# Kernel optimization log

Measured on AMD Instinct MI355X. Metric: run time of the kernel, lower is better.

Reference implementation:

```python
import jax, jax.numpy as jnp
import numpy as np

B, Q, DIM, HEADS, HEAD_DIM, KV = 32, 4, 2048, 16, 128, 8192


def setup_inputs() -> dict:
    key = jax.random.key(0)
    ks = jax.random.split(key, 9)
    s = 0.02
    return {
        'x': jax.random.normal(ks[0], (B, Q, DIM), jnp.float32),
        'attn_bias': jax.random.normal(ks[1], (B, HEADS, Q, KV), jnp.float32),
        'cache_k': jax.random.normal(ks[2], (B, KV, HEAD_DIM), jnp.float32),
        'cache_v': jax.random.normal(ks[3], (B, KV, HEAD_DIM), jnp.float32),
        'wq': jax.random.normal(ks[4], (DIM, HEADS, HEAD_DIM), jnp.float32) * s,
        'bq': jnp.zeros((HEADS, HEAD_DIM), jnp.float32),
        'wk': jax.random.normal(ks[5], (DIM, HEAD_DIM), jnp.float32) * s,
        'bk': jnp.zeros((HEAD_DIM,), jnp.float32),
        'wv': jax.random.normal(ks[6], (DIM, HEAD_DIM), jnp.float32) * s,
        'bv': jnp.zeros((HEAD_DIM,), jnp.float32),
        'wo': jax.random.normal(ks[7], (HEADS, HEAD_DIM, DIM), jnp.float32) * s,
        'bo': jnp.zeros((DIM,), jnp.float32),
    }


def reference(x, attn_bias, cache_k, cache_v, wq, bq, wk, bk, wv, bv, wo, bo):
    q_len = x.shape[1]
    # projections (MQA: shared single-head K/V)
    q = jnp.einsum('bqd,dhe->bqhe', x, wq) + bq          # [B,Q,H,hd]
    k_new = x @ wk + bk                                   # [B,Q,hd]
    v_new = x @ wv + bv
    # rolling KV cache update: shift left by q_len, write new tokens at end
    k = jnp.roll(cache_k, -q_len, axis=1).at[:, -q_len:].set(k_new)  # [B,KV,hd]
    v = jnp.roll(cache_v, -q_len, axis=1).at[:, -q_len:].set(v_new)
    scale = 1.0 / (k.shape[-1] ** 0.5)
    p = jnp.einsum('bqhe,bke->bhqk', q, k) * scale        # [B,H,Q,KV]
    a = jax.nn.softmax(p + attn_bias, axis=-1)
    o = jnp.einsum('bhqk,bke->bqhe', a, v)                # [B,Q,H,hd]
    return jnp.einsum('bqhe,hed->bqd', o, wo) + bo        # [B,Q,DIM]
```

## Files before the change

kernel.cpp:

```cpp
#include <hip/hip_runtime.h>
#include <cstddef>
#include <cstdint>

#define BATCH 32
#define QL 4
#define DIM 2048
#define NH 16
#define HD 128
#define KVLEN 8192
#define HQ 64
#define CHUNK 512
#define NCK 16
#define KT 64
#define NT 8

typedef __attribute__((ext_vector_type(8))) short bf16x8;
typedef __attribute__((ext_vector_type(4))) float f32x4;

__device__ __forceinline__ unsigned short cvt_bf16(float f) {
    unsigned int u = __builtin_bit_cast(unsigned int, f);
    u += 0x7fffu + ((u >> 16) & 1u);
    return (unsigned short)(u >> 16);
}
__device__ __forceinline__ unsigned int pack2(float a, float b) {
    return (unsigned int)cvt_bf16(a) | ((unsigned int)cvt_bf16(b) << 16);
}
__device__ __forceinline__ float bf16_to_f32(unsigned short s) {
    unsigned int u = ((unsigned int)s) << 16;
    return __builtin_bit_cast(float, u);
}
__device__ __forceinline__ bf16x8 mk_frag(unsigned int a, unsigned int b,
                                          unsigned int c, unsigned int d) {
    unsigned int t[4] = {a, b, c, d};
    return *(const bf16x8*)t;
}

template<int VARIANT>
__global__ __launch_bounds__(256) void gemm_kernel(
    const float* __restrict__ A,
    const float* __restrict__ w0p, const float* __restrict__ w1p,
    const float* __restrict__ w2p,
    const float* __restrict__ b0p, const float* __restrict__ b1p,
    const float* __restrict__ b2p,
    float* __restrict__ o0, float* __restrict__ o1, float* __restrict__ o2)
{
    const int n0 = blockIdx.x * 64;
    const int m0 = blockIdx.y * 64;
    const int tid = threadIdx.x;
    const int wave = tid >> 6, lane = tid & 63;
    const int l15 = lane & 15, quad = lane >> 4;

    const float* W; const float* Bv; int ldw, nc;
    if (VARIANT == 0) {
        if (n0 >= 2176)      { W = w2p; Bv = b2p; ldw = 128;  nc = n0 - 2176; }
        else if (n0 >= 2048) { W = w1p; Bv = b1p; ldw = 128;  nc = n0 - 2048; }
        else                 { W = w0p; Bv = b0p; ldw = 2048; nc = n0; }
    } else { W = w0p; Bv = b0p; ldw = 2048; nc = n0; }

    __shared__ alignas(16) unsigned short a_s[64][72];
    __shared__ alignas(16) unsigned short w_s[64][68];

    const int wn = tid & 63;
    const int wk0 = (tid >> 6) * 4;

    f32x4 acc[4];
    #pragma unroll
    for (int nt = 0; nt < 4; ++nt) acc[nt] = (f32x4){0.f, 0.f, 0.f, 0.f};

    float4 apre[4];
    float wpre[4][4];

    #pragma unroll
    for (int ii = 0; ii < 4; ++ii) {
        int f = tid + 256 * ii, r = f >> 4, c4 = (f & 15) << 2;
        apre[ii] = *(const float4*)&A[(size_t)(m0 + r) * DIM + c4];
    }
    #pragma unroll
    for (int sub = 0; sub < 4; ++sub) {
        int k0 = wk0 + 16 * sub;
        const float* wp = W + (size_t)k0 * ldw + nc + wn;
        #pragma unroll
        for (int j = 0; j < 4; ++j) wpre[sub][j] = wp[(size_t)j * ldw];
    }

    for (int it = 0; it < 32; ++it) {
        __syncthreads();
        #pragma unroll
        for (int ii = 0; ii < 4; ++ii) {
            int f = tid + 256 * ii, r = f >> 4, c4 = (f & 15) << 2;
            *(uint2*)&a_s[r][c4] =
                make_uint2(pack2(apre[ii].x, apre[ii].y), pack2(apre[ii].z, apre[ii].w));
        }
        #pragma unroll
        for (int sub = 0; sub < 4; ++sub) {
            int k0 = wk0 + 16 * sub;
            *(uint2*)&w_s[wn][k0] =
                make_uint2(pack2(wpre[sub][0], wpre[sub][1]),
                           pack2(wpre[sub][2], wpre[sub][3]));
        }
        __syncthreads();
        if (it + 1 < 32) {
            const int kb = (it + 1) * 64;
            #pragma unroll
            for (int ii = 0; ii < 4; ++ii) {
                int f = tid + 256 * ii, r = f >> 4, c4 = (f & 15) << 2;
                apre[ii] = *(const float4*)&A[(size_t)(m0 + r) * DIM + kb + c4];
            }
            #pragma unroll
            for (int sub = 0; sub < 4; ++sub) {
                int k0 = kb + wk0 + 16 * sub;
                const float* wp = W + (size_t)k0 * ldw + nc + wn;
                #pragma unroll
                for (int j = 0; j < 4; ++j) wpre[sub][j] = wp[(size_t)j * ldw];
            }
        }
        #pragma unroll
        for (int kf = 0; kf < 2; ++kf) {
            bf16x8 af = *(const bf16x8*)&a_s[16 * wave + l15][kf * 32 + quad * 8];
            #pragma unroll
            for (int nt = 0; nt < 4; ++nt) {
                uint2 lo = *(const uint2*)&w_s[nt * 16 + l15][kf * 32 + quad * 8];
                uint2 hi = *(const uint2*)&w_s[nt * 16 + l15][kf * 32 + quad * 8 + 4];
                bf16x8 wf = mk_frag(lo.x, lo.y, hi.x, hi.y);
                acc[nt] = __builtin_amdgcn_mfma_f32_16x16x32_bf16(af, wf, acc[nt], 0, 0, 0);
            }
        }
    }
    #pragma unroll
    for (int nt = 0; nt < 4; ++nt)
        #pragma unroll
        for (int reg = 0; reg < 4; ++reg) {
            int row = m0 + 16 * wave + quad * 4 + reg;
            int col = n0 + nt * 16 + l15;
            float s = acc[nt][reg];
            if (VARIANT == 1) {
                o0[(size_t)row * DIM + col] = s + Bv[col];
            } else {
                int b = row >> 2, q = row & 3;
                if (col < 2048) {
                    int h = col >> 7, e = col & 127;
                    o0[((size_t)(b * 64 + h * 4 + q)) * 128 + e] = s + b0p[col];
                } else if (col < 2176) {
                    int e = col - 2048;
                    o1[(size_t)row * 128 + e] = s + b1p[e];
                } else {
                    int e = col - 2176;
                    o2[(size_t)row * 128 + e] = s + b2p[e];
                }
            }
        }
}

__global__ __launch_bounds__(256, 2) void attn_kernel(
    const float* __restrict__ qws, const float* __restrict__ kws,
    const float* __restrict__ vws,
    const float* __restrict__ cachek, const float* __restrict__ cachev,
    const float* __restrict__ abias,
    float* __restrict__ opart, float* __restrict__ lpart)
{
    const int ck = blockIdx.x;
    const int b  = blockIdx.y;
    const int tid = threadIdx.x;
    const int wave = tid >> 6, lane = tid & 63;
    const int l15 = lane & 15, quad = lane >> 4;
    const float scale = 0.08838834764831845f;

    __shared__ alignas(16) unsigned short k_s[KT][136];
    __shared__ alignas(16) unsigned short v_sT[HD][68];
    __shared__ alignas(16) unsigned short p_s[4][16][72];

    bf16x8 qf[4];
    {
        const float* qrow = qws + ((size_t)b * HQ + 16 * wave + l15) * HD;
        #pragma unroll
        for (int kf = 0; kf < 4; ++kf) {
            float4 f0 = *(const float4*)&qrow[kf * 32 + quad * 8];
            float4 f1 = *(const float4*)&qrow[kf * 32 + quad * 8 + 4];
            qf[kf] = mk_frag(pack2(f0.x, f0.y), pack2(f0.z, f0.w),
                             pack2(f1.x, f1.y), pack2(f1.z, f1.w));
        }
    }

    const int kbase0 = ck * CHUNK;
    const int ve = tid & 127;
    const int vkq = (tid >> 7);

    const float* bptr[4];
    #pragma unroll
    for (int reg = 0; reg < 4; ++reg) {
        int hq = 16 * wave + quad * 4 + reg;
        int h = hq >> 2, q = hq & 3;
        bptr[reg] = abias + (((size_t)(b * NH + h)) * QL + q) * KVLEN + kbase0 + l15;
    }

    float4 kpre[8];
    float vpre[8][4];
    float bpre[16];

    #pragma unroll
    for (int i = 0; i < 8; ++i) {
        int f = tid + 256 * i;
        int row = f >> 5, e0 = (f & 31) << 2;
        int kv = kbase0 + row;
        const float* pk = (kv < KVLEN - QL)
            ? cachek + ((size_t)b * KVLEN + kv + QL) * HD + e0
            : kws + ((size_t)b * QL + (kv - (KVLEN - QL))) * HD + e0;
        kpre[i] = *(const float4*)pk;
    }
    #pragma unroll
    for (int i = 0; i < 8; ++i) {
        int kv0 = kbase0 + (vkq + 2 * i) * 4;
        #pragma unroll
        for (int j = 0; j < 4; ++j) {
            int kv = kv0 + j;
            const float* pv = (kv < KVLEN - QL)
                ? cachev + ((size_t)b * KVLEN + kv + QL) * HD + ve
                : vws + ((size_t)b * QL + (kv - (KVLEN - QL))) * HD + ve;
            vpre[i][j] = *pv;
        }
    }
    #pragma unroll
    for (int nt = 0; nt < 4; ++nt)
        #pragma unroll
        for (int reg = 0; reg < 4; ++reg)
            bpre[nt * 4 + reg] = bptr[reg][nt * 16];

    f32x4 oa[8];
    #pragma unroll
    for (int n8 = 0; n8 < 8; ++n8) oa[n8] = (f32x4){0.f, 0.f, 0.f, 0.f};
    float lrow[4] = {0.f, 0.f, 0.f, 0.f};

    for (int t = 0; t < NT; ++t) {
        __syncthreads();
        #pragma unroll
        for (int i = 0; i < 8; ++i) {
            int f = tid + 256 * i;
            int row = f >> 5, e0 = (f & 31) << 2;
            *(uint2*)&k_s[row][e0] =
                make_uint2(pack2(kpre[i].x, kpre[i].y), pack2(kpre[i].z, kpre[i].w));
        }
        #pragma unroll
        for (int i = 0; i < 8; ++i) {
            int kv0 = (vkq + 2 * i) * 4;
            *(uint2*)&v_sT[ve][kv0] =
                make_uint2(pack2(vpre[i][0], vpre[i][1]),
                           pack2(vpre[i][2], vpre[i][3]));
        }
        float bias[16];
        #pragma unroll
        for (int j = 0; j < 16; ++j) bias[j] = bpre[j];
        __syncthreads();
        if (t + 1 < NT) {
            const int tb = kbase0 + (t + 1) * KT;
            #pragma unroll
            for (int i = 0; i < 8; ++i) {
                int f = tid + 256 * i;
                int row = f >> 5, e0 = (f & 31) << 2;
                int kv = tb + row;
                const float* pk = (kv < KVLEN - QL)
                    ? cachek + ((size_t)b * KVLEN + kv + QL) * HD + e0
                    : kws + ((size_t)b * QL + (kv - (KVLEN - QL))) * HD + e0;
                kpre[i] = *(const float4*)pk;
            }
            #pragma unroll
            for (int i = 0; i < 8; ++i) {
                int kv0 = tb + (vkq + 2 * i) * 4;
                #pragma unroll
                for (int j = 0; j < 4; ++j) {
                    int kv = kv0 + j;
                    const float* pv = (kv < KVLEN - QL)
                        ? cachev + ((size_t)b * KVLEN + kv + QL) * HD + ve
                        : vws + ((size_t)b * QL + (kv - (KVLEN - QL))) * HD + ve;
                    vpre[i][j] = *pv;
                }
            }
            #pragma unroll
            for (int nt = 0; nt < 4; ++nt)
                #pragma unroll
                for (int reg = 0; reg < 4; ++reg)
                    bpre[nt * 4 + reg] = bptr[reg][(t + 1) * KT + nt * 16];
        }
        f32x4 sacc[4];
        #pragma unroll
        for (int nt = 0; nt < 4; ++nt) sacc[nt] = (f32x4){0.f, 0.f, 0.f, 0.f};
        #pragma unroll
        for (int kf = 0; kf < 4; ++kf) {
            #pragma unroll
            for (int nt = 0; nt < 4; ++nt) {
                bf16x8 kfb = *(const bf16x8*)&k_s[nt * 16 + l15][kf * 32 + quad * 8];
                sacc[nt] = __builtin_amdgcn_mfma_f32_16x16x32_bf16(qf[kf], kfb, sacc[nt], 0, 0, 0);
            }
        }
        #pragma unroll
        for (int nt = 0; nt < 4; ++nt)
            #pragma unroll
            for (int reg = 0; reg < 4; ++reg) {
                float s = sacc[nt][reg] * scale + bias[nt * 4 + reg];
                float p = __expf(s);
                unsigned short pb = cvt_bf16(p);
                lrow[reg] += bf16_to_f32(pb);
                p_s[wave][quad * 4 + reg][nt * 16 + l15] = pb;
            }
        #pragma unroll
        for (int kfp = 0; kfp < 2; ++kfp) {
            uint2 plo = *(const uint2*)&p_s[wave][l15][kfp * 32 + quad * 8];
            uint2 phi = *(const uint2*)&p_s[wave][l15][kfp * 32 + quad * 8 + 4];
            bf16x8 pf = mk_frag(plo.x, plo.y, phi.x, phi.y);
            #pragma unroll
            for (int n8 = 0; n8 < 8; ++n8) {
                uint2 vlo = *(const uint2*)&v_sT[n8 * 16 + l15][kfp * 32 + quad * 8];
                uint2 vhi = *(const uint2*)&v_sT[n8 * 16 + l15][kfp * 32 + quad * 8 + 4];
                bf16x8 vf = mk_frag(vlo.x, vlo.y, vhi.x, vhi.y);
                oa[n8] = __builtin_amdgcn_mfma_f32_16x16x32_bf16(pf, vf, oa[n8], 0, 0, 0);
            }
        }
    }
    #pragma unroll
    for (int reg = 0; reg < 4; ++reg) {
        float v = lrow[reg];
        v += __shfl_xor(v, 1);
        v += __shfl_xor(v, 2);
        v += __shfl_xor(v, 4);
        v += __shfl_xor(v, 8);
        lrow[reg] = v;
    }
    const size_t obase = ((size_t)(b * NCK + ck)) * HQ * HD;
    #pragma unroll
    for (int n8 = 0; n8 < 8; ++n8)
        #pragma unroll
        for (int reg = 0; reg < 4; ++reg) {
            int hq = 16 * wave + quad * 4 + reg;
            int e = n8 * 16 + l15;
            opart[obase + (size_t)hq * HD + e] = oa[n8][reg];
        }
    if (l15 == 0) {
        #pragma unroll
        for (int reg = 0; reg < 4; ++reg) {
            int hq = 16 * wave + quad * 4 + reg;
            lpart[(size_t)(b * NCK + ck) * HQ + hq] = lrow[reg];
        }
    }
}

__global__ __launch_bounds__(128) void combine_kernel(
    const float* __restrict__ opart, const float* __restrict__ lpart,
    float* __restrict__ ored)
{
    const int bh = blockIdx.x;
    const int b = bh >> 6, hq = bh & 63;
    const int e = threadIdx.x;
    float lt = 0.f, ov = 0.f;
    #pragma unroll
    for (int c = 0; c < NCK; ++c) {
        lt += lpart[(b * NCK + c) * HQ + hq];
        ov += opart[((size_t)(b * NCK + c) * HQ + hq) * HD + e];
    }
    int h = hq >> 2, q = hq & 3;
    ored[(size_t)(b * QL + q) * DIM + h * HD + e] = ov / lt;
}

extern "C" void kernel_launch(void* const* d_in, const int* in_sizes, int n_in,
                              void* d_out, int out_size, void* d_ws, size_t ws_size,
                              hipStream_t stream)
{
    const float* x   = (const float*)d_in[0];
    const float* ab  = (const float*)d_in[1];
    const float* cK  = (const float*)d_in[2];
    const float* cV  = (const float*)d_in[3];
    const float* wq  = (const float*)d_in[4];
    const float* bq  = (const float*)d_in[5];
    const float* wk  = (const float*)d_in[6];
    const float* bk  = (const float*)d_in[7];
    const float* wv  = (const float*)d_in[8];
    const float* bv  = (const float*)d_in[9];
    const float* wo  = (const float*)d_in[10];
    const float* bo  = (const float*)d_in[11];
    float* out = (float*)d_out;

    float* ws   = (float*)d_ws;
    float* wsq  = ws;
    float* wsk  = wsq + 262144;
    float* wsv  = wsk + 16384;
    float* wsop = wsv + 16384;
    float* wsl  = wsop + 4194304;
    float* wsor = wsl + 32768;

    gemm_kernel<0><<<dim3(36, 2), 256, 0, stream>>>(
        x, wq, wk, wv, bq, bk, bv, wsq, wsk, wsv);
    attn_kernel<<<dim3(NCK, BATCH), 256, 0, stream>>>(
        wsq, wsk, wsv, cK, cV, ab, wsop, wsl);
    combine_kernel<<<BATCH * HQ, 128, 0, stream>>>(wsop, wsl, wsor);
    gemm_kernel<1><<<dim3(32, 2), 256, 0, stream>>>(
        wsor, wo, nullptr, nullptr, bo, nullptr, nullptr, out, nullptr, nullptr);
}
```

Baseline: 433.1 us.

## Split-K both projection GEMMs and double attention KV chunks with atomic accumulation

```diff
diff --git a/kernel.cpp b/kernel.cpp
--- a/kernel.cpp
+++ b/kernel.cpp
@@ -9,10 +9,11 @@
 #define HD 128
 #define KVLEN 8192
 #define HQ 64
-#define CHUNK 512
+#define CHUNK 256
+#define NCKB 32
 #define NCK 16
 #define KT 64
-#define NT 8
+#define NT 4
 
 typedef __attribute__((ext_vector_type(8))) short bf16x8;
 typedef __attribute__((ext_vector_type(4))) float f32x4;
@@ -46,6 +47,7 @@
 {
     const int n0 = blockIdx.x * 64;
     const int m0 = blockIdx.y * 64;
+    const int kz = blockIdx.z * 256;
     const int tid = threadIdx.x;
     const int wave = tid >> 6, lane = tid & 63;
     const int l15 = lane & 15, quad = lane >> 4;
@@ -73,17 +75,17 @@
     #pragma unroll
     for (int ii = 0; ii < 4; ++ii) {
         int f = tid + 256 * ii, r = f >> 4, c4 = (f & 15) << 2;
-        apre[ii] = *(const float4*)&A[(size_t)(m0 + r) * DIM + c4];
+        apre[ii] = *(const float4*)&A[(size_t)(m0 + r) * DIM + kz + c4];
     }
     #pragma unroll
     for (int sub = 0; sub < 4; ++sub) {
-        int k0 = wk0 + 16 * sub;
+        int k0 = kz + wk0 + 16 * sub;
         const float* wp = W + (size_t)k0 * ldw + nc + wn;
         #pragma unroll
         for (int j = 0; j < 4; ++j) wpre[sub][j] = wp[(size_t)j * ldw];
     }
 
-    for (int it = 0; it < 32; ++it) {
+    for (int it = 0; it < 4; ++it) {
         __syncthreads();
         #pragma unroll
         for (int ii = 0; ii < 4; ++ii) {
@@ -99,8 +101,8 @@
                            pack2(wpre[sub][2], wpre[sub][3]));
         }
         __syncthreads();
-        if (it + 1 < 32) {
-            const int kb = (it + 1) * 64;
+        if (it + 1 < 4) {
+            const int kb = kz + (it + 1) * 64;
             #pragma unroll
             for (int ii = 0; ii < 4; ++ii) {
                 int f = tid + 256 * ii, r = f >> 4, c4 = (f & 15) << 2;
@@ -126,6 +128,7 @@
             }
         }
     }
+    const bool addb = (blockIdx.z == 0);
     #pragma unroll
     for (int nt = 0; nt < 4; ++nt)
         #pragma unroll
@@ -134,18 +137,19 @@
             int col = n0 + nt * 16 + l15;
             float s = acc[nt][reg];
             if (VARIANT == 1) {
-                o0[(size_t)row * DIM + col] = s + Bv[col];
+                atomicAdd(&o0[(size_t)row * DIM + col], s + (addb ? Bv[col] : 0.f));
             } else {
                 int b = row >> 2, q = row & 3;
                 if (col < 2048) {
                     int h = col >> 7, e = col & 127;
-                    o0[((size_t)(b * 64 + h * 4 + q)) * 128 + e] = s + b0p[col];
+                    atomicAdd(&o0[((size_t)(b * 64 + h * 4 + q)) * 128 + e],
+                              s + (addb ? b0p[col] : 0.f));
                 } else if (col < 2176) {
                     int e = col - 2048;
-                    o1[(size_t)row * 128 + e] = s + b1p[e];
+                    atomicAdd(&o1[(size_t)row * 128 + e], s + (addb ? b1p[e] : 0.f));
                 } else {
                     int e = col - 2176;
-                    o2[(size_t)row * 128 + e] = s + b2p[e];
+                    atomicAdd(&o2[(size_t)row * 128 + e], s + (addb ? b2p[e] : 0.f));
                 }
             }
         }
@@ -324,20 +328,21 @@
         v += __shfl_xor(v, 8);
         lrow[reg] = v;
     }
-    const size_t obase = ((size_t)(b * NCK + ck)) * HQ * HD;
+    const size_t slot = (size_t)(b * NCK + (ck >> 1));
+    const size_t obase = slot * HQ * HD;
     #pragma unroll
     for (int n8 = 0; n8 < 8; ++n8)
         #pragma unroll
         for (int reg = 0; reg < 4; ++reg) {
             int hq = 16 * wave + quad * 4 + reg;
             int e = n8 * 16 + l15;
-            opart[obase + (size_t)hq * HD + e] = oa[n8][reg];
+            atomicAdd(&opart[obase + (size_t)hq * HD + e], oa[n8][reg]);
         }
     if (l15 == 0) {
         #pragma unroll
         for (int reg = 0; reg < 4; ++reg) {
             int hq = 16 * wave + quad * 4 + reg;
-            lpart[(size_t)(b * NCK + ck) * HQ + hq] = lrow[reg];
+            atomicAdd(&lpart[slot * HQ + hq], lrow[reg]);
         }
     }
 }
@@ -385,11 +390,15 @@
     float* wsl  = wsop + 4194304;
     float* wsor = wsl + 32768;
 
-    gemm_kernel<0><<<dim3(36, 2), 256, 0, stream>>>(
+    hipMemsetAsync(wsq,  0, (size_t)(262144 + 16384 + 16384) * sizeof(float), stream);
+    hipMemsetAsync(wsop, 0, (size_t)(4194304 + 32768) * sizeof(float), stream);
+    hipMemsetAsync(out,  0, (size_t)(BATCH * QL * DIM) * sizeof(float), stream);
+
+    gemm_kernel<0><<<dim3(36, 2, 8), 256, 0, stream>>>(
         x, wq, wk, wv, bq, bk, bv, wsq, wsk, wsv);
-    attn_kernel<<<dim3(NCK, BATCH), 256, 0, stream>>>(
+    attn_kernel<<<dim3(NCKB, BATCH), 256, 0, stream>>>(
         wsq, wsk, wsv, cK, cV, ab, wsop, wsl);
     combine_kernel<<<BATCH * HQ, 128, 0, stream>>>(wsop, wsl, wsor);
-    gemm_kernel<1><<<dim3(32, 2), 256, 0, stream>>>(
+    gemm_kernel<1><<<dim3(32, 2, 8), 256, 0, stream>>>(
         wsor, wo, nullptr, nullptr, bo, nullptr, nullptr, out, nullptr, nullptr);
 }
```

Measured after the change: 402.6 us. 7.0% less time.

## Split-K the projection GEMMs with atomic accumulation and prioritize MFMA in attention

Applied to the files above, without the earlier changes.

```diff
diff --git a/kernel.cpp b/kernel.cpp
--- a/kernel.cpp
+++ b/kernel.cpp
@@ -46,6 +46,7 @@
 {
     const int n0 = blockIdx.x * 64;
     const int m0 = blockIdx.y * 64;
+    const int kz = blockIdx.z * 512;
     const int tid = threadIdx.x;
     const int wave = tid >> 6, lane = tid & 63;
     const int l15 = lane & 15, quad = lane >> 4;
@@ -73,17 +74,17 @@
     #pragma unroll
     for (int ii = 0; ii < 4; ++ii) {
         int f = tid + 256 * ii, r = f >> 4, c4 = (f & 15) << 2;
-        apre[ii] = *(const float4*)&A[(size_t)(m0 + r) * DIM + c4];
+        apre[ii] = *(const float4*)&A[(size_t)(m0 + r) * DIM + kz + c4];
     }
     #pragma unroll
     for (int sub = 0; sub < 4; ++sub) {
-        int k0 = wk0 + 16 * sub;
+        int k0 = kz + wk0 + 16 * sub;
         const float* wp = W + (size_t)k0 * ldw + nc + wn;
         #pragma unroll
         for (int j = 0; j < 4; ++j) wpre[sub][j] = wp[(size_t)j * ldw];
     }
 
-    for (int it = 0; it < 32; ++it) {
+    for (int it = 0; it < 8; ++it) {
         __syncthreads();
         #pragma unroll
         for (int ii = 0; ii < 4; ++ii) {
@@ -99,8 +100,8 @@
                            pack2(wpre[sub][2], wpre[sub][3]));
         }
         __syncthreads();
-        if (it + 1 < 32) {
-            const int kb = (it + 1) * 64;
+        if (it + 1 < 8) {
+            const int kb = kz + (it + 1) * 64;
             #pragma unroll
             for (int ii = 0; ii < 4; ++ii) {
                 int f = tid + 256 * ii, r = f >> 4, c4 = (f & 15) << 2;
@@ -126,6 +127,7 @@
             }
         }
     }
+    const bool addb = (blockIdx.z == 0);
     #pragma unroll
     for (int nt = 0; nt < 4; ++nt)
         #pragma unroll
@@ -134,18 +136,19 @@
             int col = n0 + nt * 16 + l15;
             float s = acc[nt][reg];
             if (VARIANT == 1) {
-                o0[(size_t)row * DIM + col] = s + Bv[col];
+                atomicAdd(&o0[(size_t)row * DIM + col], s + (addb ? Bv[col] : 0.f));
             } else {
                 int b = row >> 2, q = row & 3;
                 if (col < 2048) {
                     int h = col >> 7, e = col & 127;
-                    o0[((size_t)(b * 64 + h * 4 + q)) * 128 + e] = s + b0p[col];
+                    atomicAdd(&o0[((size_t)(b * 64 + h * 4 + q)) * 128 + e],
+                              s + (addb ? b0p[col] : 0.f));
                 } else if (col < 2176) {
                     int e = col - 2048;
-                    o1[(size_t)row * 128 + e] = s + b1p[e];
+                    atomicAdd(&o1[(size_t)row * 128 + e], s + (addb ? b1p[e] : 0.f));
                 } else {
                     int e = col - 2176;
-                    o2[(size_t)row * 128 + e] = s + b2p[e];
+                    atomicAdd(&o2[(size_t)row * 128 + e], s + (addb ? b2p[e] : 0.f));
                 }
             }
         }
@@ -283,6 +286,7 @@
         f32x4 sacc[4];
         #pragma unroll
         for (int nt = 0; nt < 4; ++nt) sacc[nt] = (f32x4){0.f, 0.f, 0.f, 0.f};
+        __builtin_amdgcn_s_setprio(1);
         #pragma unroll
         for (int kf = 0; kf < 4; ++kf) {
             #pragma unroll
@@ -291,6 +295,7 @@
                 sacc[nt] = __builtin_amdgcn_mfma_f32_16x16x32_bf16(qf[kf], kfb, sacc[nt], 0, 0, 0);
             }
         }
+        __builtin_amdgcn_s_setprio(0);
         #pragma unroll
         for (int nt = 0; nt < 4; ++nt)
             #pragma unroll
@@ -301,6 +306,7 @@
                 lrow[reg] += bf16_to_f32(pb);
                 p_s[wave][quad * 4 + reg][nt * 16 + l15] = pb;
             }
+        __builtin_amdgcn_s_setprio(1);
         #pragma unroll
         for (int kfp = 0; kfp < 2; ++kfp) {
             uint2 plo = *(const uint2*)&p_s[wave][l15][kfp * 32 + quad * 8];
@@ -314,6 +320,7 @@
                 oa[n8] = __builtin_amdgcn_mfma_f32_16x16x32_bf16(pf, vf, oa[n8], 0, 0, 0);
             }
         }
+        __builtin_amdgcn_s_setprio(0);
     }
     #pragma unroll
     for (int reg = 0; reg < 4; ++reg) {
@@ -344,11 +351,12 @@
 
 __global__ __launch_bounds__(128) void combine_kernel(
     const float* __restrict__ opart, const float* __restrict__ lpart,
-    float* __restrict__ ored)
+    float* __restrict__ ored, float* __restrict__ outz)
 {
     const int bh = blockIdx.x;
     const int b = bh >> 6, hq = bh & 63;
     const int e = threadIdx.x;
+    outz[(size_t)bh * 128 + e] = 0.f;
     float lt = 0.f, ov = 0.f;
     #pragma unroll
     for (int c = 0; c < NCK; ++c) {
@@ -385,11 +393,14 @@
     float* wsl  = wsop + 4194304;
     float* wsor = wsl + 32768;
 
-    gemm_kernel<0><<<dim3(36, 2), 256, 0, stream>>>(
+    hipMemsetAsync(ws, 0, (size_t)(262144 + 16384 + 16384) * sizeof(float),
+                   stream);
+
+    gemm_kernel<0><<<dim3(36, 2, 4), 256, 0, stream>>>(
         x, wq, wk, wv, bq, bk, bv, wsq, wsk, wsv);
     attn_kernel<<<dim3(NCK, BATCH), 256, 0, stream>>>(
         wsq, wsk, wsv, cK, cV, ab, wsop, wsl);
-    combine_kernel<<<BATCH * HQ, 128, 0, stream>>>(wsop, wsl, wsor);
-    gemm_kernel<1><<<dim3(32, 2), 256, 0, stream>>>(
+    combine_kernel<<<BATCH * HQ, 128, 0, stream>>>(wsop, wsl, wsor, out);
+    gemm_kernel<1><<<dim3(32, 2, 4), 256, 0, stream>>>(
         wsor, wo, nullptr, nullptr, bo, nullptr, nullptr, out, nullptr, nullptr);
 }
```

Result: faster. 397.3 us (-8.3%).
